# Kernel tuning notes

Hardware: AMD Instinct MI355X
Metric: run time of the kernel (lower is better)

## Reference

```python
import jax, jax.numpy as jnp
import numpy as np

DIM = 512
HEADS = 8
DIM_HEAD = 64
INNER = HEADS * DIM_HEAD


def setup_inputs() -> dict:
    key = jax.random.key(0)
    k1, k2, k3, k4 = jax.random.split(key, 4)
    x = jax.random.normal(k1, (4, 8192, DIM), dtype=jnp.float32)
    # nn.Linear(dim, inner*3, bias=False): weight applied as x @ W^T; store transposed form [dim, 3*inner]
    w_qkv = jax.random.normal(k2, (DIM, 3 * INNER), dtype=jnp.float32) / np.sqrt(DIM)
    w_out = jax.random.normal(k3, (INNER, DIM), dtype=jnp.float32) / np.sqrt(INNER)
    b_out = jax.random.normal(k4, (DIM,), dtype=jnp.float32) * 0.01
    return {"x": x, "w_qkv": w_qkv, "w_out": w_out, "b_out": b_out}


def reference(x, w_qkv, w_out, b_out):
    b, n, d = x.shape
    qkv = x @ w_qkv  # [b, n, 3*inner]
    q, k, v = jnp.split(qkv, 3, axis=-1)

    def to_heads(t):
        return t.reshape(b, n, HEADS, DIM_HEAD).transpose(0, 2, 1, 3)  # [b,h,n,dh]

    q, k, v = map(to_heads, (q, k, v))
    q = jax.nn.elu(q) + 1.0
    k = jax.nn.elu(k) + 1.0
    # kv summary: [b,h,dh,dh]
    kv = jnp.einsum('bhnd,bhnm->bhdm', k, v)
    # normalizer z: [b,h,n]  (note: original does NOT apply self.scale)
    z = 1.0 / (jnp.einsum('bhnd,bhd->bhn', q, k.sum(axis=2)) + 1e-6)
    out = jnp.einsum('bhnd,bhdm->bhnm', q, kv) * z[..., None]  # [b,h,n,dh]
    out = out.transpose(0, 2, 1, 3).reshape(b, n, INNER)
    return out @ w_out + b_out
```

## Files before the change

kernel.cpp:

```cpp
#include <hip/hip_runtime.h>
#include <hip/hip_bf16.h>

#define B_SZ 4
#define SEQ 8192
#define DIM 512
#define HEADS 8
#define DH 64
#define INNER 512
#define QKV_COLS 1536
#define M_TOT (B_SZ * SEQ)
#define BHN (B_SZ * HEADS)

typedef __bf16 bf16x8 __attribute__((ext_vector_type(8)));
typedef __bf16 bf16x4 __attribute__((ext_vector_type(4)));
typedef float f32x4 __attribute__((ext_vector_type(4)));

__device__ __forceinline__ float elu1(float x) {
    return x > 0.f ? x + 1.f : __expf(x);
}

__device__ __forceinline__ void gl_lds16(const void* g, void* l) {
    __builtin_amdgcn_global_load_lds(
        (const __attribute__((address_space(1))) unsigned int*)g,
        (__attribute__((address_space(3))) unsigned int*)l, 16, 0, 0);
}

__global__ void convert_all(const float* __restrict__ x,
                            const float* __restrict__ w_qkv,
                            const float* __restrict__ w_out,
                            __bf16* __restrict__ xb,
                            __bf16* __restrict__ wqkv_t,
                            __bf16* __restrict__ wout_t) {
    const int NX = M_TOT * DIM / 4;
    int id = blockIdx.x * 256 + threadIdx.x;
    if (id < NX) {
        float4 f = reinterpret_cast<const float4*>(x)[id];
        bf16x4 h = {(__bf16)f.x, (__bf16)f.y, (__bf16)f.z, (__bf16)f.w};
        reinterpret_cast<bf16x4*>(xb)[id] = h;
        return;
    }
    int id2 = id - NX;
    if (id2 < QKV_COLS * DIM) {
        int n = id2 / DIM, k = id2 % DIM;
        wqkv_t[id2] = (__bf16)w_qkv[k * QKV_COLS + n];
    } else {
        int id3 = id2 - QKV_COLS * DIM;
        if (id3 < INNER * DIM) {
            int n = id3 / DIM, k = id3 % DIM;
            wout_t[id3] = (__bf16)w_out[k * DIM + n];
        }
    }
}

#define TSTR 136
__launch_bounds__(256, 2)
__global__ void gemm_qkv(const __bf16* __restrict__ xb,
                         const __bf16* __restrict__ wqkv_t,
                         __bf16* __restrict__ q_ws,
                         __bf16* __restrict__ kT_ws,
                         __bf16* __restrict__ vT_ws) {
    __shared__ __attribute__((aligned(16))) char smem[128 * TSTR * 2];
    __bf16* As = (__bf16*)smem;
    __bf16* Bs = (__bf16*)(smem + 16384);
    __bf16* T  = (__bf16*)smem;

    const int tid = threadIdx.x;
    const int wid = tid >> 6;
    const int lane = tid & 63;
    const int wm = wid >> 1, wn = wid & 1;
    const int lq = lane >> 4, lr = lane & 15;
    const int m0 = blockIdx.x * 128;
    const int n0 = blockIdx.y * 128;
    const int lrow = lane >> 3;
    const int lsw  = ((lane & 7) ^ lrow) * 8;

    f32x4 acc[4][4] = {};

    for (int kb = 0; kb < DIM; kb += 64) {
#pragma unroll
        for (int t = 0; t < 4; ++t) {
            int qi = wid * 4 + t;
            int row = qi * 8 + lrow;
            gl_lds16(&xb[(size_t)(m0 + row) * DIM + kb + lsw], &As[qi * 512]);
            gl_lds16(&wqkv_t[(size_t)(n0 + row) * DIM + kb + lsw], &Bs[qi * 512]);
        }
        __syncthreads();
#pragma unroll
        for (int ks = 0; ks < 2; ++ks) {
            const int csw = ((ks * 4 + lq) ^ (lr & 7)) * 8;
            bf16x8 af[4], bfv[4];
#pragma unroll
            for (int i = 0; i < 4; ++i)
                af[i] = *reinterpret_cast<const bf16x8*>(
                    &As[(wm * 64 + i * 16 + lr) * 64 + csw]);
#pragma unroll
            for (int j = 0; j < 4; ++j)
                bfv[j] = *reinterpret_cast<const bf16x8*>(
                    &Bs[(wn * 64 + j * 16 + lr) * 64 + csw]);
#pragma unroll
            for (int i = 0; i < 4; ++i)
#pragma unroll
                for (int j = 0; j < 4; ++j)
                    acc[i][j] = __builtin_amdgcn_mfma_f32_16x16x32_bf16(
                        af[i], bfv[j], acc[i][j], 0, 0, 0);
        }
        __syncthreads();
    }

    const int which = n0 / INNER;
    const int n0w = n0 % INNER;
    const int b = m0 / SEQ;
    const int nbase = m0 % SEQ;

    if (which == 0) {
#pragma unroll
        for (int i = 0; i < 4; ++i)
#pragma unroll
            for (int j = 0; j < 4; ++j) {
                int col = wn * 64 + j * 16 + lr;
#pragma unroll
                for (int r = 0; r < 4; ++r)
                    T[(wm * 64 + i * 16 + lq * 4 + r) * TSTR + col] =
                        (__bf16)elu1(acc[i][j][r]);
            }
        __syncthreads();
#pragma unroll
        for (int it = 0; it < 8; ++it) {
            int c = tid + it * 256;
            int row = c >> 4, dc = (c & 15) * 8;
            bf16x8 v = *reinterpret_cast<const bf16x8*>(&T[row * TSTR + dc]);
            int col = n0w + dc;
            int h = col >> 6, d = col & 63;
            *reinterpret_cast<bf16x8*>(
                &q_ws[(((size_t)(b * HEADS + h)) * SEQ + nbase + row) * DH + d]) = v;
        }
    } else {
        __bf16* dst = (which == 1) ? kT_ws : vT_ws;
#pragma unroll
        for (int i = 0; i < 4; ++i)
#pragma unroll
            for (int j = 0; j < 4; ++j) {
                int col = wn * 64 + j * 16 + lr;
                int rowb = wm * 64 + i * 16 + lq * 4;
                bf16x4 h4;
#pragma unroll
                for (int r = 0; r < 4; ++r) {
                    float v = acc[i][j][r];
                    h4[r] = (__bf16)((which == 1) ? elu1(v) : v);
                }
                *reinterpret_cast<bf16x4*>(&T[col * TSTR + rowb]) = h4;
            }
        __syncthreads();
#pragma unroll
        for (int it = 0; it < 8; ++it) {
            int c = tid + it * 256;
            int colIdx = c >> 4, rc = (c & 15) * 8;
            bf16x8 v = *reinterpret_cast<const bf16x8*>(&T[colIdx * TSTR + rc]);
            int gcol = n0w + colIdx;
            int h = gcol >> 6, d = gcol & 63;
            *reinterpret_cast<bf16x8*>(
                &dst[(((size_t)(b * HEADS + h)) * DH + d) * SEQ + nbase + rc]) = v;
        }
    }
}

__launch_bounds__(256, 2)
__global__ void kv_reduce(const __bf16* __restrict__ kT,
                          const __bf16* __restrict__ vT,
                          float* __restrict__ kv_t,
                          float* __restrict__ ksum) {
    __shared__ __attribute__((aligned(16))) __bf16 Ks[64][136];
    __shared__ __attribute__((aligned(16))) __bf16 Vs[64][136];
    const int tid = threadIdx.x;
    const int wid = tid >> 6;
    const int lane = tid & 63;
    const int lq = lane >> 4, lr = lane & 15;
    const int bh = blockIdx.y;
    const int n0 = blockIdx.x * 512;
    const size_t base = (size_t)bh * DH * SEQ;
    f32x4 acc[4] = {};
    f32x4 acc1 = {};
    bf16x8 ones8;
#pragma unroll
    for (int e = 0; e < 8; ++e) ones8[e] = (__bf16)1.f;

    for (int ch = 0; ch < 4; ++ch) {
        int nc = n0 + ch * 128;
#pragma unroll
        for (int t = 0; t < 4; ++t) {
            int c = tid + t * 256;
            int row = c >> 4, kc = (c & 15) * 8;
            *reinterpret_cast<bf16x8*>(&Ks[row][kc]) =
                *reinterpret_cast<const bf16x8*>(&kT[base + (size_t)row * SEQ + nc + kc]);
            *reinterpret_cast<bf16x8*>(&Vs[row][kc]) =
                *reinterpret_cast<const bf16x8*>(&vT[base + (size_t)row * SEQ + nc + kc]);
        }
        __syncthreads();
#pragma unroll
        for (int ks = 0; ks < 4; ++ks) {
            bf16x8 a = *reinterpret_cast<const bf16x8*>(&Ks[wid * 16 + lr][ks * 32 + lq * 8]);
            acc1 = __builtin_amdgcn_mfma_f32_16x16x32_bf16(a, ones8, acc1, 0, 0, 0);
#pragma unroll
            for (int j = 0; j < 4; ++j) {
                bf16x8 b = *reinterpret_cast<const bf16x8*>(&Vs[j * 16 + lr][ks * 32 + lq * 8]);
                acc[j] = __builtin_amdgcn_mfma_f32_16x16x32_bf16(a, b, acc[j], 0, 0, 0);
            }
        }
        __syncthreads();
    }
    float* dst = kv_t + (size_t)bh * DH * DH;
#pragma unroll
    for (int j = 0; j < 4; ++j) {
        int m = j * 16 + lr;
#pragma unroll
        for (int r = 0; r < 4; ++r) {
            int d = wid * 16 + lq * 4 + r;
            atomicAdd(&dst[m * DH + d], acc[j][r]);
        }
    }
    if (lr == 0) {
#pragma unroll
        for (int r = 0; r < 4; ++r)
            atomicAdd(&ksum[bh * DH + wid * 16 + lq * 4 + r], acc1[r]);
    }
}

__launch_bounds__(256, 2)
__global__ void attn_kernel(const __bf16* __restrict__ q_ws,
                            const float* __restrict__ kv_t,
                            const float* __restrict__ ksum,
                            __bf16* __restrict__ attn) {
    __shared__ __attribute__((aligned(16))) __bf16 Qs[128][72];
    __shared__ __attribute__((aligned(16))) __bf16 KVs[64][72];
    __shared__ float zs[128];
    __shared__ float ks_s[64];
    const int tid = threadIdx.x;
    const int wid = tid >> 6, lane = tid & 63;
    const int lq = lane >> 4, lr = lane & 15;
    const int bh = blockIdx.y;
    const int b = bh >> 3, h = bh & 7;
    const int n0 = blockIdx.x * 128;
    const size_t qbase = ((size_t)bh * SEQ + n0) * DH;

#pragma unroll
    for (int t = 0; t < 4; ++t) {
        int c = tid + t * 256;
        int row = c >> 3, kc = (c & 7) * 8;
        *reinterpret_cast<bf16x8*>(&Qs[row][kc]) =
            *reinterpret_cast<const bf16x8*>(&q_ws[qbase + (size_t)row * DH + kc]);
    }
    const float* kvsrc = kv_t + (size_t)bh * DH * DH;
#pragma unroll
    for (int t = 0; t < 4; ++t) {
        int c = tid + t * 256;
        int m = c >> 4, dc = (c & 15) * 4;
        float4 f = *reinterpret_cast<const float4*>(&kvsrc[m * DH + dc]);
        bf16x4 h4 = {(__bf16)f.x, (__bf16)f.y, (__bf16)f.z, (__bf16)f.w};
        *reinterpret_cast<bf16x4*>(&KVs[m][dc]) = h4;
    }
    if (tid < 64) ks_s[tid] = ksum[bh * DH + tid];
    __syncthreads();
    {
        int row = tid >> 1, part = tid & 1;
        float s = 0.f;
#pragma unroll
        for (int j = 0; j < 32; ++j)
            s += (float)Qs[row][part * 32 + j] * ks_s[part * 32 + j];
        s += __shfl_xor(s, 1, 64);
        if (part == 0) zs[row] = 1.f / (s + 1e-6f);
    }
    __syncthreads();

    f32x4 acc[2][4] = {};
#pragma unroll
    for (int ks = 0; ks < 2; ++ks) {
        bf16x8 a0 = *reinterpret_cast<const bf16x8*>(&Qs[wid * 32 + lr][ks * 32 + lq * 8]);
        bf16x8 a1 = *reinterpret_cast<const bf16x8*>(&Qs[wid * 32 + 16 + lr][ks * 32 + lq * 8]);
#pragma unroll
        for (int j = 0; j < 4; ++j) {
            bf16x8 bfr = *reinterpret_cast<const bf16x8*>(&KVs[j * 16 + lr][ks * 32 + lq * 8]);
            acc[0][j] = __builtin_amdgcn_mfma_f32_16x16x32_bf16(a0, bfr, acc[0][j], 0, 0, 0);
            acc[1][j] = __builtin_amdgcn_mfma_f32_16x16x32_bf16(a1, bfr, acc[1][j], 0, 0, 0);
        }
    }
    __syncthreads();
#pragma unroll
    for (int mt = 0; mt < 2; ++mt)
#pragma unroll
        for (int j = 0; j < 4; ++j) {
            int m = j * 16 + lr;
#pragma unroll
            for (int r = 0; r < 4; ++r) {
                int row = wid * 32 + mt * 16 + lq * 4 + r;
                Qs[row][m] = (__bf16)(acc[mt][j][r] * zs[row]);
            }
        }
    __syncthreads();
#pragma unroll
    for (int it = 0; it < 4; ++it) {
        int c = tid + it * 256;
        int row = c >> 3, mc = (c & 7) * 8;
        bf16x8 v = *reinterpret_cast<const bf16x8*>(&Qs[row][mc]);
        *reinterpret_cast<bf16x8*>(
            &attn[((size_t)(b * SEQ + n0 + row)) * INNER + h * DH + mc]) = v;
    }
}

__launch_bounds__(256, 2)
__global__ void gemm_out(const __bf16* __restrict__ attn,
                         const __bf16* __restrict__ wout_t,
                         const float* __restrict__ b_out,
                         float* __restrict__ out) {
    __shared__ __attribute__((aligned(16))) char smem[32768];
    __bf16* As = (__bf16*)smem;
    __bf16* Bs = (__bf16*)(smem + 16384);

    const int tid = threadIdx.x;
    const int wid = tid >> 6;
    const int lane = tid & 63;
    const int wm = wid >> 1, wn = wid & 1;
    const int lq = lane >> 4, lr = lane & 15;
    const int m0 = blockIdx.x * 128;
    const int n0 = blockIdx.y * 128;
    const int lrow = lane >> 3;
    const int lsw  = ((lane & 7) ^ lrow) * 8;

    f32x4 acc[4][4] = {};

    for (int kb = 0; kb < INNER; kb += 64) {
#pragma unroll
        for (int t = 0; t < 4; ++t) {
            int qi = wid * 4 + t;
            int row = qi * 8 + lrow;
            gl_lds16(&attn[(size_t)(m0 + row) * INNER + kb + lsw], &As[qi * 512]);
            gl_lds16(&wout_t[(size_t)(n0 + row) * INNER + kb + lsw], &Bs[qi * 512]);
        }
        __syncthreads();
#pragma unroll
        for (int ks = 0; ks < 2; ++ks) {
            const int csw = ((ks * 4 + lq) ^ (lr & 7)) * 8;
            bf16x8 af[4], bfv[4];
#pragma unroll
            for (int i = 0; i < 4; ++i)
                af[i] = *reinterpret_cast<const bf16x8*>(
                    &As[(wm * 64 + i * 16 + lr) * 64 + csw]);
#pragma unroll
            for (int j = 0; j < 4; ++j)
                bfv[j] = *reinterpret_cast<const bf16x8*>(
                    &Bs[(wn * 64 + j * 16 + lr) * 64 + csw]);
#pragma unroll
            for (int i = 0; i < 4; ++i)
#pragma unroll
                for (int j = 0; j < 4; ++j)
                    acc[i][j] = __builtin_amdgcn_mfma_f32_16x16x32_bf16(
                        af[i], bfv[j], acc[i][j], 0, 0, 0);
        }
        __syncthreads();
    }

#pragma unroll
    for (int j = 0; j < 4; ++j) {
        int col = n0 + wn * 64 + j * 16 + lr;
        float bias = b_out[col];
#pragma unroll
        for (int i = 0; i < 4; ++i) {
            int row = m0 + wm * 64 + i * 16 + lq * 4;
#pragma unroll
            for (int r = 0; r < 4; ++r)
                out[(size_t)(row + r) * DIM + col] = acc[i][j][r] + bias;
        }
    }
}

extern "C" void kernel_launch(void* const* d_in, const int* in_sizes, int n_in,
                              void* d_out, int out_size, void* d_ws, size_t ws_size,
                              hipStream_t stream) {
    (void)in_sizes; (void)n_in; (void)out_size; (void)ws_size;
    const float* x     = (const float*)d_in[0];
    const float* w_qkv = (const float*)d_in[1];
    const float* w_out = (const float*)d_in[2];
    const float* b_out = (const float*)d_in[3];
    float* out = (float*)d_out;

    char* ws = (char*)d_ws;
    size_t off = 0;
    auto alloc = [&](size_t bytes) {
        char* p = ws + off;
        off += (bytes + 255) & ~(size_t)255;
        return p;
    };
    __bf16* xb     = (__bf16*)alloc((size_t)M_TOT * DIM * 2);
    __bf16* attn   = xb;
    __bf16* q_ws   = (__bf16*)alloc((size_t)BHN * SEQ * DH * 2);
    __bf16* kT_ws  = (__bf16*)alloc((size_t)BHN * SEQ * DH * 2);
    __bf16* vT_ws  = (__bf16*)alloc((size_t)BHN * SEQ * DH * 2);
    float*  kv_t   = (float*)alloc((size_t)BHN * DH * DH * 4 + (size_t)BHN * DH * 4);
    float*  ksum   = kv_t + (size_t)BHN * DH * DH;
    __bf16* wqkv_t = (__bf16*)alloc((size_t)QKV_COLS * DIM * 2);
    __bf16* wout_t = (__bf16*)alloc((size_t)INNER * DIM * 2);

    hipMemsetAsync(kv_t, 0, (size_t)BHN * DH * DH * 4 + (size_t)BHN * DH * 4, stream);
    convert_all<<<dim3(M_TOT * DIM / 4 / 256 + (QKV_COLS * DIM + INNER * DIM) / 256),
                  256, 0, stream>>>(x, w_qkv, w_out, xb, wqkv_t, wout_t);
    gemm_qkv<<<dim3(M_TOT / 128, QKV_COLS / 128), 256, 0, stream>>>(
        xb, wqkv_t, q_ws, kT_ws, vT_ws);
    kv_reduce<<<dim3(16, BHN), 256, 0, stream>>>(kT_ws, vT_ws, kv_t, ksum);
    attn_kernel<<<dim3(SEQ / 128, BHN), 256, 0, stream>>>(q_ws, kv_t, ksum, attn);
    gemm_out<<<dim3(M_TOT / 128, DIM / 128), 256, 0, stream>>>(attn, wout_t, b_out, out);
}
```

Before: 284.2 us.

## Rewrite QKV and output GEMMs as 256x256 double-buffered pipelined tiles

```diff
diff --git a/kernel.cpp b/kernel.cpp
--- a/kernel.cpp
+++ b/kernel.cpp
@@ -24,6 +24,9 @@
         (const __attribute__((address_space(1))) unsigned int*)g,
         (__attribute__((address_space(3))) unsigned int*)l, 16, 0, 0);
 }
+
+#define MFMA16(a, b, c) __builtin_amdgcn_mfma_f32_16x16x32_bf16(a, b, c, 0, 0, 0)
+#define BARRIER() asm volatile("s_barrier" ::: "memory")
 
 __global__ void convert_all(const float* __restrict__ x,
                             const float* __restrict__ w_qkv,
@@ -52,114 +55,229 @@
     }
 }
 
+__device__ __forceinline__ void gemm256_core(
+    const __bf16* __restrict__ Am, const __bf16* __restrict__ Bm,
+    int m0, int n0, char* smem, f32x4 acc[8][4])
+{
+    const int tid = threadIdx.x;
+    const int wid = tid >> 6;
+    const int lane = tid & 63;
+    const int wm = wid >> 2, wn = wid & 3;
+    const int lq = lane >> 4, lr = lane & 15;
+    const int lrow = lane >> 3;
+    const int lsw  = ((lane & 7) ^ lrow) * 8;
+
+    __bf16* const As0 = (__bf16*)smem;
+    __bf16* const Bs0 = (__bf16*)(smem + 32768);
+    __bf16* const As1 = (__bf16*)(smem + 65536);
+    __bf16* const Bs1 = (__bf16*)(smem + 98304);
+
+    const int csw0 = ((0 + lq) ^ (lr & 7)) * 8;
+    const int csw1 = ((4 + lq) ^ (lr & 7)) * 8;
+
+    auto stageB = [&](__bf16* Bs, int kt, int u) {
+        gl_lds16(&Bm[(size_t)(n0 + u * 64 + wid * 8 + lrow) * 512 + kt * 64 + lsw],
+                 Bs + (u * 64 + wid * 8) * 64);
+    };
+    auto stageA = [&](__bf16* As, int kt, int s2) {
+        int gr = (wid < 4) ? (s2 * 32 + wid * 8) : (128 + s2 * 32 + (wid - 4) * 8);
+        gl_lds16(&Am[(size_t)(m0 + gr + lrow) * 512 + kt * 64 + lsw],
+                 As + gr * 64);
+    };
+    auto ldA = [&](const __bf16* As, int m, int csw) -> bf16x8 {
+        return *reinterpret_cast<const bf16x8*>(As + (wm * 128 + m * 16 + lr) * 64 + csw);
+    };
+    auto ldB = [&](const __bf16* Bs, int n, int csw) -> bf16x8 {
+        return *reinterpret_cast<const bf16x8*>(Bs + (wn * 64 + n * 16 + lr) * 64 + csw);
+    };
+
+    stageB(Bs0, 0, 0); stageB(Bs0, 0, 1); stageB(Bs0, 0, 2); stageB(Bs0, 0, 3);
+    stageA(As0, 0, 0); stageA(As0, 0, 1); stageA(As0, 0, 2); stageA(As0, 0, 3);
+    asm volatile("s_waitcnt vmcnt(3)" ::: "memory");
+    BARRIER();
+
+#pragma unroll 2
+    for (int t = 0; t < 8; ++t) {
+        __bf16* const As  = (t & 1) ? As1 : As0;
+        __bf16* const Bs  = (t & 1) ? Bs1 : Bs0;
+        __bf16* const Asn = (t & 1) ? As0 : As1;
+        __bf16* const Bsn = (t & 1) ? Bs0 : Bs1;
+        const bool pf = (t < 7);
+        bf16x8 bfr[4][2];
+
+        {
+            bf16x8 a00 = ldA(As, 0, csw0), a01 = ldA(As, 0, csw1);
+            bf16x8 a10 = ldA(As, 1, csw0), a11 = ldA(As, 1, csw1);
+#pragma unroll
+            for (int n = 0; n < 4; ++n) { bfr[n][0] = ldB(Bs, n, csw0); bfr[n][1] = ldB(Bs, n, csw1); }
+            if (pf) { stageB(Bsn, t + 1, 0); stageB(Bsn, t + 1, 1); }
+            __builtin_amdgcn_s_setprio(1);
+#pragma unroll
+            for (int n = 0; n < 4; ++n) {
+                acc[0][n] = MFMA16(a00, bfr[n][0], acc[0][n]);
+                acc[0][n] = MFMA16(a01, bfr[n][1], acc[0][n]);
+                acc[1][n] = MFMA16(a10, bfr[n][0], acc[1][n]);
+                acc[1][n] = MFMA16(a11, bfr[n][1], acc[1][n]);
+            }
+            __builtin_amdgcn_s_setprio(0);
+            if (pf) asm volatile("s_waitcnt vmcnt(4)" ::: "memory");
+            else    asm volatile("s_waitcnt vmcnt(2)" ::: "memory");
+            BARRIER();
+        }
+        {
+            bf16x8 a00 = ldA(As, 2, csw0), a01 = ldA(As, 2, csw1);
+            bf16x8 a10 = ldA(As, 3, csw0), a11 = ldA(As, 3, csw1);
+            if (pf) { stageB(Bsn, t + 1, 2); stageB(Bsn, t + 1, 3); }
+            __builtin_amdgcn_s_setprio(1);
+#pragma unroll
+            for (int n = 0; n < 4; ++n) {
+                acc[2][n] = MFMA16(a00, bfr[n][0], acc[2][n]);
+                acc[2][n] = MFMA16(a01, bfr[n][1], acc[2][n]);
+                acc[3][n] = MFMA16(a10, bfr[n][0], acc[3][n]);
+                acc[3][n] = MFMA16(a11, bfr[n][1], acc[3][n]);
+            }
+            __builtin_amdgcn_s_setprio(0);
+            if (pf) asm volatile("s_waitcnt vmcnt(5)" ::: "memory");
+            else    asm volatile("s_waitcnt vmcnt(1)" ::: "memory");
+            BARRIER();
+        }
+        {
+            bf16x8 a00 = ldA(As, 4, csw0), a01 = ldA(As, 4, csw1);
+            bf16x8 a10 = ldA(As, 5, csw0), a11 = ldA(As, 5, csw1);
+            if (pf) { stageA(Asn, t + 1, 0); stageA(Asn, t + 1, 1); }
+            __builtin_amdgcn_s_setprio(1);
+#pragma unroll
+            for (int n = 0; n < 4; ++n) {
+                acc[4][n] = MFMA16(a00, bfr[n][0], acc[4][n]);
+                acc[4][n] = MFMA16(a01, bfr[n][1], acc[4][n]);
+                acc[5][n] = MFMA16(a10, bfr[n][0], acc[5][n]);
+                acc[5][n] = MFMA16(a11, bfr[n][1], acc[5][n]);
+            }
+            __builtin_amdgcn_s_setprio(0);
+            if (pf) asm volatile("s_waitcnt vmcnt(6)" ::: "memory");
+            else    asm volatile("s_waitcnt vmcnt(0)" ::: "memory");
+            BARRIER();
+        }
+        {
+            bf16x8 a00 = ldA(As, 6, csw0), a01 = ldA(As, 6, csw1);
+            bf16x8 a10 = ldA(As, 7, csw0), a11 = ldA(As, 7, csw1);
+            if (pf) { stageA(Asn, t + 1, 2); stageA(Asn, t + 1, 3); }
+            __builtin_amdgcn_s_setprio(1);
+#pragma unroll
+            for (int n = 0; n < 4; ++n) {
+                acc[6][n] = MFMA16(a00, bfr[n][0], acc[6][n]);
+                acc[6][n] = MFMA16(a01, bfr[n][1], acc[6][n]);
+                acc[7][n] = MFMA16(a10, bfr[n][0], acc[7][n]);
+                acc[7][n] = MFMA16(a11, bfr[n][1], acc[7][n]);
+            }
+            __builtin_amdgcn_s_setprio(0);
+            if (pf) asm volatile("s_waitcnt vmcnt(3)" ::: "memory");
+            BARRIER();
+        }
+    }
+}
+
 #define TSTR 136
-__launch_bounds__(256, 2)
+__launch_bounds__(512, 2)
 __global__ void gemm_qkv(const __bf16* __restrict__ xb,
                          const __bf16* __restrict__ wqkv_t,
                          __bf16* __restrict__ q_ws,
                          __bf16* __restrict__ kT_ws,
                          __bf16* __restrict__ vT_ws) {
-    __shared__ __attribute__((aligned(16))) char smem[128 * TSTR * 2];
-    __bf16* As = (__bf16*)smem;
-    __bf16* Bs = (__bf16*)(smem + 16384);
-    __bf16* T  = (__bf16*)smem;
+    __shared__ __attribute__((aligned(16))) char smem[131072];
+    const int f  = blockIdx.y * gridDim.x + blockIdx.x;
+    const int xc = f & 7, sl = f >> 3;
+    const int m0 = (xc * 16 + sl / 6) * 256;
+    const int n0 = (sl % 6) * 256;
+
+    f32x4 acc[8][4] = {};
+    gemm256_core(xb, wqkv_t, m0, n0, smem, acc);
 
     const int tid = threadIdx.x;
     const int wid = tid >> 6;
     const int lane = tid & 63;
-    const int wm = wid >> 1, wn = wid & 1;
+    const int wm = wid >> 2, wn = wid & 3;
     const int lq = lane >> 4, lr = lane & 15;
-    const int m0 = blockIdx.x * 128;
-    const int n0 = blockIdx.y * 128;
-    const int lrow = lane >> 3;
-    const int lsw  = ((lane & 7) ^ lrow) * 8;
-
-    f32x4 acc[4][4] = {};
-
-    for (int kb = 0; kb < DIM; kb += 64) {
-#pragma unroll
-        for (int t = 0; t < 4; ++t) {
-            int qi = wid * 4 + t;
-            int row = qi * 8 + lrow;
-            gl_lds16(&xb[(size_t)(m0 + row) * DIM + kb + lsw], &As[qi * 512]);
-            gl_lds16(&wqkv_t[(size_t)(n0 + row) * DIM + kb + lsw], &Bs[qi * 512]);
-        }
-        __syncthreads();
-#pragma unroll
-        for (int ks = 0; ks < 2; ++ks) {
-            const int csw = ((ks * 4 + lq) ^ (lr & 7)) * 8;
-            bf16x8 af[4], bfv[4];
-#pragma unroll
-            for (int i = 0; i < 4; ++i)
-                af[i] = *reinterpret_cast<const bf16x8*>(
-                    &As[(wm * 64 + i * 16 + lr) * 64 + csw]);
-#pragma unroll
-            for (int j = 0; j < 4; ++j)
-                bfv[j] = *reinterpret_cast<const bf16x8*>(
-                    &Bs[(wn * 64 + j * 16 + lr) * 64 + csw]);
-#pragma unroll
-            for (int i = 0; i < 4; ++i)
-#pragma unroll
-                for (int j = 0; j < 4; ++j)
-                    acc[i][j] = __builtin_amdgcn_mfma_f32_16x16x32_bf16(
-                        af[i], bfv[j], acc[i][j], 0, 0, 0);
-        }
-        __syncthreads();
-    }
 
     const int which = n0 / INNER;
     const int n0w = n0 % INNER;
     const int b = m0 / SEQ;
     const int nbase = m0 % SEQ;
 
+    __bf16* const T0 = (__bf16*)smem;
+    __bf16* const T1 = (__bf16*)(smem + 34816);
+
     if (which == 0) {
 #pragma unroll
-        for (int i = 0; i < 4; ++i)
-#pragma unroll
-            for (int j = 0; j < 4; ++j) {
-                int col = wn * 64 + j * 16 + lr;
-#pragma unroll
-                for (int r = 0; r < 4; ++r)
-                    T[(wm * 64 + i * 16 + lq * 4 + r) * TSTR + col] =
-                        (__bf16)elu1(acc[i][j][r]);
-            }
-        __syncthreads();
-#pragma unroll
-        for (int it = 0; it < 8; ++it) {
-            int c = tid + it * 256;
-            int row = c >> 4, dc = (c & 15) * 8;
-            bf16x8 v = *reinterpret_cast<const bf16x8*>(&T[row * TSTR + dc]);
-            int col = n0w + dc;
-            int h = col >> 6, d = col & 63;
-            *reinterpret_cast<bf16x8*>(
-                &q_ws[(((size_t)(b * HEADS + h)) * SEQ + nbase + row) * DH + d]) = v;
+        for (int rh = 0; rh < 2; ++rh) {
+            if (wm == rh) {
+#pragma unroll
+                for (int m = 0; m < 8; ++m)
+#pragma unroll
+                    for (int n = 0; n < 4; ++n) {
+                        int col = wn * 64 + n * 16 + lr;
+                        __bf16* Tb = (wn * 64 + n * 16 < 128) ? T0 : T1;
+                        int cl = col & 127;
+#pragma unroll
+                        for (int r = 0; r < 4; ++r)
+                            Tb[(m * 16 + lq * 4 + r) * TSTR + cl] =
+                                (__bf16)elu1(acc[m][n][r]);
+                    }
+            }
+            __syncthreads();
+#pragma unroll
+            for (int it = 0; it < 8; ++it) {
+                int cch = tid + it * 512;
+                int row = cch >> 5;
+                int cc = (cch & 31) * 8;
+                const __bf16* Tb = (cc < 128) ? T0 : T1;
+                int dc = cc & 127;
+                bf16x8 v = *reinterpret_cast<const bf16x8*>(&Tb[row * TSTR + dc]);
+                int colg = n0w + cc;
+                int h = colg >> 6, d = colg & 63;
+                *reinterpret_cast<bf16x8*>(
+                    &q_ws[(((size_t)(b * HEADS + h)) * SEQ + nbase + rh * 128 + row) * DH + d]) = v;
+            }
+            __syncthreads();
         }
     } else {
         __bf16* dst = (which == 1) ? kT_ws : vT_ws;
 #pragma unroll
-        for (int i = 0; i < 4; ++i)
-#pragma unroll
-            for (int j = 0; j < 4; ++j) {
-                int col = wn * 64 + j * 16 + lr;
-                int rowb = wm * 64 + i * 16 + lq * 4;
-                bf16x4 h4;
-#pragma unroll
-                for (int r = 0; r < 4; ++r) {
-                    float v = acc[i][j][r];
-                    h4[r] = (__bf16)((which == 1) ? elu1(v) : v);
+        for (int rh = 0; rh < 2; ++rh) {
+            if (wm == rh) {
+#pragma unroll
+                for (int m = 0; m < 8; ++m) {
+                    int rowb = m * 16 + lq * 4;
+#pragma unroll
+                    for (int n = 0; n < 4; ++n) {
+                        int col = wn * 64 + n * 16 + lr;
+                        __bf16* Tb = (wn * 64 + n * 16 < 128) ? T0 : T1;
+                        int cl = col & 127;
+                        bf16x4 h4;
+#pragma unroll
+                        for (int r = 0; r < 4; ++r) {
+                            float v = acc[m][n][r];
+                            h4[r] = (__bf16)((which == 1) ? elu1(v) : v);
+                        }
+                        *reinterpret_cast<bf16x4*>(&Tb[cl * TSTR + rowb]) = h4;
+                    }
                 }
-                *reinterpret_cast<bf16x4*>(&T[col * TSTR + rowb]) = h4;
-            }
-        __syncthreads();
-#pragma unroll
-        for (int it = 0; it < 8; ++it) {
-            int c = tid + it * 256;
-            int colIdx = c >> 4, rc = (c & 15) * 8;
-            bf16x8 v = *reinterpret_cast<const bf16x8*>(&T[colIdx * TSTR + rc]);
-            int gcol = n0w + colIdx;
-            int h = gcol >> 6, d = gcol & 63;
-            *reinterpret_cast<bf16x8*>(
-                &dst[(((size_t)(b * HEADS + h)) * DH + d) * SEQ + nbase + rc]) = v;
+            }
+            __syncthreads();
+#pragma unroll
+            for (int it = 0; it < 8; ++it) {
+                int cch = tid + it * 512;
+                int colIdx = cch >> 4;
+                int rc = (cch & 15) * 8;
+                const __bf16* Tb = (colIdx < 128) ? T0 : T1;
+                int cl = colIdx & 127;
+                bf16x8 v = *reinterpret_cast<const bf16x8*>(&Tb[cl * TSTR + rc]);
+                int g = n0w + colIdx;
+                int h = g >> 6, d = g & 63;
+                *reinterpret_cast<bf16x8*>(
+                    &dst[(((size_t)(b * HEADS + h)) * DH + d) * SEQ + nbase + rh * 128 + rc]) = v;
+            }
+            __syncthreads();
         }
     }
 }
@@ -199,11 +317,11 @@
 #pragma unroll
         for (int ks = 0; ks < 4; ++ks) {
             bf16x8 a = *reinterpret_cast<const bf16x8*>(&Ks[wid * 16 + lr][ks * 32 + lq * 8]);
-            acc1 = __builtin_amdgcn_mfma_f32_16x16x32_bf16(a, ones8, acc1, 0, 0, 0);
+            acc1 = MFMA16(a, ones8, acc1);
 #pragma unroll
             for (int j = 0; j < 4; ++j) {
                 bf16x8 b = *reinterpret_cast<const bf16x8*>(&Vs[j * 16 + lr][ks * 32 + lq * 8]);
-                acc[j] = __builtin_amdgcn_mfma_f32_16x16x32_bf16(a, b, acc[j], 0, 0, 0);
+                acc[j] = MFMA16(a, b, acc[j]);
             }
         }
         __syncthreads();
@@ -279,8 +397,8 @@
 #pragma unroll
         for (int j = 0; j < 4; ++j) {
             bf16x8 bfr = *reinterpret_cast<const bf16x8*>(&KVs[j * 16 + lr][ks * 32 + lq * 8]);
-            acc[0][j] = __builtin_amdgcn_mfma_f32_16x16x32_bf16(a0, bfr, acc[0][j], 0, 0, 0);
-            acc[1][j] = __builtin_amdgcn_mfma_f32_16x16x32_bf16(a1, bfr, acc[1][j], 0, 0, 0);
+            acc[0][j] = MFMA16(a0, bfr, acc[0][j]);
+            acc[1][j] = MFMA16(a1, bfr, acc[1][j]);
         }
     }
     __syncthreads();
@@ -306,68 +424,36 @@
     }
 }
 
-__launch_bounds__(256, 2)
+__launch_bounds__(512, 2)
 __global__ void gemm_out(const __bf16* __restrict__ attn,
                          const __bf16* __restrict__ wout_t,
                          const float* __restrict__ b_out,
                          float* __restrict__ out) {
-    __shared__ __attribute__((aligned(16))) char smem[32768];
-    __bf16* As = (__bf16*)smem;
-    __bf16* Bs = (__bf16*)(smem + 16384);
+    __shared__ __attribute__((aligned(16))) char smem[131072];
+    const int f  = blockIdx.y * gridDim.x + blockIdx.x;
+    const int xc = f & 7, sl = f >> 3;
+    const int m0 = (xc * 16 + (sl >> 1)) * 256;
+    const int n0 = (sl & 1) * 256;
+
+    f32x4 acc[8][4] = {};
+    gemm256_core(attn, wout_t, m0, n0, smem, acc);
 
     const int tid = threadIdx.x;
     const int wid = tid >> 6;
     const int lane = tid & 63;
-    const int wm = wid >> 1, wn = wid & 1;
+    const int wm = wid >> 2, wn = wid & 3;
     const int lq = lane >> 4, lr = lane & 15;
-    const int m0 = blockIdx.x * 128;
-    const int n0 = blockIdx.y * 128;
-    const int lrow = lane >> 3;
-    const int lsw  = ((lane & 7) ^ lrow) * 8;
-
-    f32x4 acc[4][4] = {};
-
-    for (int kb = 0; kb < INNER; kb += 64) {
-#pragma unroll
-        for (int t = 0; t < 4; ++t) {
-            int qi = wid * 4 + t;
-            int row = qi * 8 + lrow;
-            gl_lds16(&attn[(size_t)(m0 + row) * INNER + kb + lsw], &As[qi * 512]);
-            gl_lds16(&wout_t[(size_t)(n0 + row) * INNER + kb + lsw], &Bs[qi * 512]);
-        }
-        __syncthreads();
-#pragma unroll
-        for (int ks = 0; ks < 2; ++ks) {
-            const int csw = ((ks * 4 + lq) ^ (lr & 7)) * 8;
-            bf16x8 af[4], bfv[4];
-#pragma unroll
-            for (int i = 0; i < 4; ++i)
-                af[i] = *reinterpret_cast<const bf16x8*>(
-                    &As[(wm * 64 + i * 16 + lr) * 64 + csw]);
-#pragma unroll
-            for (int j = 0; j < 4; ++j)
-                bfv[j] = *reinterpret_cast<const bf16x8*>(
-                    &Bs[(wn * 64 + j * 16 + lr) * 64 + csw]);
-#pragma unroll
-            for (int i = 0; i < 4; ++i)
-#pragma unroll
-                for (int j = 0; j < 4; ++j)
-                    acc[i][j] = __builtin_amdgcn_mfma_f32_16x16x32_bf16(
-                        af[i], bfv[j], acc[i][j], 0, 0, 0);
-        }
-        __syncthreads();
-    }
-
-#pragma unroll
-    for (int j = 0; j < 4; ++j) {
-        int col = n0 + wn * 64 + j * 16 + lr;
+
+#pragma unroll
+    for (int n = 0; n < 4; ++n) {
+        int col = n0 + wn * 64 + n * 16 + lr;
         float bias = b_out[col];
 #pragma unroll
-        for (int i = 0; i < 4; ++i) {
-            int row = m0 + wm * 64 + i * 16 + lq * 4;
+        for (int m = 0; m < 8; ++m) {
+            int row = m0 + wm * 128 + m * 16 + lq * 4;
 #pragma unroll
             for (int r = 0; r < 4; ++r)
-                out[(size_t)(row + r) * DIM + col] = acc[i][j][r] + bias;
+                out[(size_t)(row + r) * DIM + col] = acc[m][n][r] + bias;
         }
     }
 }
@@ -402,9 +488,9 @@
     hipMemsetAsync(kv_t, 0, (size_t)BHN * DH * DH * 4 + (size_t)BHN * DH * 4, stream);
     convert_all<<<dim3(M_TOT * DIM / 4 / 256 + (QKV_COLS * DIM + INNER * DIM) / 256),
                   256, 0, stream>>>(x, w_qkv, w_out, xb, wqkv_t, wout_t);
-    gemm_qkv<<<dim3(M_TOT / 128, QKV_COLS / 128), 256, 0, stream>>>(
+    gemm_qkv<<<dim3(M_TOT / 256, QKV_COLS / 256), 512, 0, stream>>>(
         xb, wqkv_t, q_ws, kT_ws, vT_ws);
     kv_reduce<<<dim3(16, BHN), 256, 0, stream>>>(kT_ws, vT_ws, kv_t, ksum);
     attn_kernel<<<dim3(SEQ / 128, BHN), 256, 0, stream>>>(q_ws, kv_t, ksum, attn);
-    gemm_out<<<dim3(M_TOT / 128, DIM / 128), 256, 0, stream>>>(attn, wout_t, b_out, out);
-}
+    gemm_out<<<dim3(M_TOT / 256, DIM / 256), 512, 0, stream>>>(attn, wout_t, b_out, out);
+}
```

After: 269.5 us. 1.05x faster.

## Fuse attention apply with output projection in one per-row-tile kernel

Applied to the files above, without the earlier changes.

```diff
diff --git a/kernel.cpp b/kernel.cpp
--- a/kernel.cpp
+++ b/kernel.cpp
@@ -24,6 +24,8 @@
         (const __attribute__((address_space(1))) unsigned int*)g,
         (__attribute__((address_space(3))) unsigned int*)l, 16, 0, 0);
 }
+
+#define MFMA16(a, b, c) __builtin_amdgcn_mfma_f32_16x16x32_bf16(a, b, c, 0, 0, 0)
 
 __global__ void convert_all(const float* __restrict__ x,
                             const float* __restrict__ w_qkv,
@@ -101,8 +103,7 @@
             for (int i = 0; i < 4; ++i)
 #pragma unroll
                 for (int j = 0; j < 4; ++j)
-                    acc[i][j] = __builtin_amdgcn_mfma_f32_16x16x32_bf16(
-                        af[i], bfv[j], acc[i][j], 0, 0, 0);
+                    acc[i][j] = MFMA16(af[i], bfv[j], acc[i][j]);
         }
         __syncthreads();
     }
@@ -199,11 +200,11 @@
 #pragma unroll
         for (int ks = 0; ks < 4; ++ks) {
             bf16x8 a = *reinterpret_cast<const bf16x8*>(&Ks[wid * 16 + lr][ks * 32 + lq * 8]);
-            acc1 = __builtin_amdgcn_mfma_f32_16x16x32_bf16(a, ones8, acc1, 0, 0, 0);
+            acc1 = MFMA16(a, ones8, acc1);
 #pragma unroll
             for (int j = 0; j < 4; ++j) {
                 bf16x8 b = *reinterpret_cast<const bf16x8*>(&Vs[j * 16 + lr][ks * 32 + lq * 8]);
-                acc[j] = __builtin_amdgcn_mfma_f32_16x16x32_bf16(a, b, acc[j], 0, 0, 0);
+                acc[j] = MFMA16(a, b, acc[j]);
             }
         }
         __syncthreads();
@@ -225,149 +226,132 @@
     }
 }
 
-__launch_bounds__(256, 2)
-__global__ void attn_kernel(const __bf16* __restrict__ q_ws,
-                            const float* __restrict__ kv_t,
-                            const float* __restrict__ ksum,
-                            __bf16* __restrict__ attn) {
-    __shared__ __attribute__((aligned(16))) __bf16 Qs[128][72];
-    __shared__ __attribute__((aligned(16))) __bf16 KVs[64][72];
+__launch_bounds__(512, 2)
+__global__ void attn_out(const __bf16* __restrict__ q_ws,
+                         const float* __restrict__ kv_t,
+                         const float* __restrict__ ksum,
+                         const __bf16* __restrict__ wout_t,
+                         const float* __restrict__ b_out,
+                         float* __restrict__ out) {
+    __shared__ __attribute__((aligned(16))) __bf16 kvs[2][64 * 64];
+    __shared__ __attribute__((aligned(16))) __bf16 attn_lds[128 * 64];
     __shared__ float zs[128];
-    __shared__ float ks_s[64];
+
     const int tid = threadIdx.x;
     const int wid = tid >> 6, lane = tid & 63;
     const int lq = lane >> 4, lr = lane & 15;
-    const int bh = blockIdx.y;
-    const int b = bh >> 3, h = bh & 7;
-    const int n0 = blockIdx.x * 128;
-    const size_t qbase = ((size_t)bh * SEQ + n0) * DH;
-
-#pragma unroll
-    for (int t = 0; t < 4; ++t) {
-        int c = tid + t * 256;
-        int row = c >> 3, kc = (c & 7) * 8;
-        *reinterpret_cast<bf16x8*>(&Qs[row][kc]) =
-            *reinterpret_cast<const bf16x8*>(&q_ws[qbase + (size_t)row * DH + kc]);
-    }
-    const float* kvsrc = kv_t + (size_t)bh * DH * DH;
-#pragma unroll
-    for (int t = 0; t < 4; ++t) {
-        int c = tid + t * 256;
-        int m = c >> 4, dc = (c & 15) * 4;
-        float4 f = *reinterpret_cast<const float4*>(&kvsrc[m * DH + dc]);
-        bf16x4 h4 = {(__bf16)f.x, (__bf16)f.y, (__bf16)f.z, (__bf16)f.w};
-        *reinterpret_cast<bf16x4*>(&KVs[m][dc]) = h4;
-    }
-    if (tid < 64) ks_s[tid] = ksum[bh * DH + tid];
+    const int wm = wid >> 2, wn = wid & 3;
+    const int m0 = blockIdx.x * 128;
+    const int b = m0 / SEQ;
+    const int nseq = m0 % SEQ;
+
+    f32x4 acc[4][8] = {};
+
+    auto stage_kv = [&](int buf, int h) {
+        int m = tid >> 3, c0 = tid & 7;
+        const float* src = &kv_t[(((size_t)(b * 8 + h)) * 64 + m) * 64 + c0 * 8];
+        float4 f0 = *reinterpret_cast<const float4*>(src);
+        float4 f1 = *reinterpret_cast<const float4*>(src + 4);
+        bf16x8 v = {(__bf16)f0.x, (__bf16)f0.y, (__bf16)f0.z, (__bf16)f0.w,
+                    (__bf16)f1.x, (__bf16)f1.y, (__bf16)f1.z, (__bf16)f1.w};
+        *reinterpret_cast<bf16x8*>(&kvs[buf][m * 64 + ((c0 ^ (m & 7)) * 8)]) = v;
+    };
+
+    stage_kv(0, 0);
     __syncthreads();
-    {
-        int row = tid >> 1, part = tid & 1;
-        float s = 0.f;
-#pragma unroll
-        for (int j = 0; j < 32; ++j)
-            s += (float)Qs[row][part * 32 + j] * ks_s[part * 32 + j];
-        s += __shfl_xor(s, 1, 64);
-        if (part == 0) zs[row] = 1.f / (s + 1e-6f);
-    }
-    __syncthreads();
-
-    f32x4 acc[2][4] = {};
-#pragma unroll
-    for (int ks = 0; ks < 2; ++ks) {
-        bf16x8 a0 = *reinterpret_cast<const bf16x8*>(&Qs[wid * 32 + lr][ks * 32 + lq * 8]);
-        bf16x8 a1 = *reinterpret_cast<const bf16x8*>(&Qs[wid * 32 + 16 + lr][ks * 32 + lq * 8]);
-#pragma unroll
-        for (int j = 0; j < 4; ++j) {
-            bf16x8 bfr = *reinterpret_cast<const bf16x8*>(&KVs[j * 16 + lr][ks * 32 + lq * 8]);
-            acc[0][j] = __builtin_amdgcn_mfma_f32_16x16x32_bf16(a0, bfr, acc[0][j], 0, 0, 0);
-            acc[1][j] = __builtin_amdgcn_mfma_f32_16x16x32_bf16(a1, bfr, acc[1][j], 0, 0, 0);
-        }
-    }
-    __syncthreads();
-#pragma unroll
-    for (int mt = 0; mt < 2; ++mt)
-#pragma unroll
-        for (int j = 0; j < 4; ++j) {
-            int m = j * 16 + lr;
-#pragma unroll
-            for (int r = 0; r < 4; ++r) {
-                int row = wid * 32 + mt * 16 + lq * 4 + r;
-                Qs[row][m] = (__bf16)(acc[mt][j][r] * zs[row]);
+
+    for (int h = 0; h < 8; ++h) {
+        const int buf = h & 1;
+        const size_t qb = (((size_t)(b * 8 + h)) * SEQ + nseq) * DH;
+
+        {
+            int row = tid >> 2, part = tid & 3;
+            const __bf16* qp = &q_ws[qb + (size_t)row * DH + part * 16];
+            bf16x8 v0 = *reinterpret_cast<const bf16x8*>(qp);
+            bf16x8 v1 = *reinterpret_cast<const bf16x8*>(qp + 8);
+            const float* kp = &ksum[(b * 8 + h) * 64 + part * 16];
+            float s = 0.f;
+#pragma unroll
+            for (int j = 0; j < 8; ++j) s += (float)v0[j] * kp[j];
+#pragma unroll
+            for (int j = 0; j < 8; ++j) s += (float)v1[j] * kp[8 + j];
+            s += __shfl_xor(s, 1, 64);
+            s += __shfl_xor(s, 2, 64);
+            if (part == 0) zs[row] = 1.f / (s + 1e-6f);
+        }
+
+        {
+            const int r0 = wid * 16;
+            bf16x8 qa[2];
+#pragma unroll
+            for (int ks = 0; ks < 2; ++ks)
+                qa[ks] = *reinterpret_cast<const bf16x8*>(
+                    &q_ws[qb + (size_t)(r0 + lr) * DH + ks * 32 + lq * 8]);
+            f32x4 acc1[4] = {};
+#pragma unroll
+            for (int ks = 0; ks < 2; ++ks)
+#pragma unroll
+                for (int j = 0; j < 4; ++j) {
+                    int mr = j * 16 + lr;
+                    bf16x8 bk = *reinterpret_cast<const bf16x8*>(
+                        &kvs[buf][mr * 64 + (((ks * 4 + lq) ^ (mr & 7)) * 8)]);
+                    acc1[j] = MFMA16(qa[ks], bk, acc1[j]);
+                }
+            asm volatile("s_waitcnt lgkmcnt(0)" ::: "memory");
+            float zr[4];
+#pragma unroll
+            for (int r = 0; r < 4; ++r) zr[r] = zs[r0 + lq * 4 + r];
+#pragma unroll
+            for (int j = 0; j < 4; ++j)
+#pragma unroll
+                for (int r = 0; r < 4; ++r) {
+                    int row = r0 + lq * 4 + r;
+                    int chk = j * 2 + (lr >> 3);
+                    attn_lds[row * 64 + ((chk ^ (row & 7)) * 8) + (lr & 7)] =
+                        (__bf16)(acc1[j][r] * zr[r]);
+                }
+        }
+        if (h < 7) stage_kv(buf ^ 1, h + 1);
+        __syncthreads();
+
+        {
+            bf16x8 af[4][2];
+#pragma unroll
+            for (int i = 0; i < 4; ++i)
+#pragma unroll
+                for (int ks = 0; ks < 2; ++ks) {
+                    int arow = wm * 64 + i * 16 + lr;
+                    af[i][ks] = *reinterpret_cast<const bf16x8*>(
+                        &attn_lds[arow * 64 + (((ks * 4 + lq) ^ (arow & 7)) * 8)]);
+                }
+#pragma unroll
+            for (int n = 0; n < 8; ++n) {
+                int c = wn * 128 + n * 16 + lr;
+                const __bf16* wp = &wout_t[(size_t)c * 512 + h * 64 + lq * 8];
+                bf16x8 bw0 = *reinterpret_cast<const bf16x8*>(wp);
+                bf16x8 bw1 = *reinterpret_cast<const bf16x8*>(wp + 32);
+                __builtin_amdgcn_s_setprio(1);
+#pragma unroll
+                for (int i = 0; i < 4; ++i) {
+                    acc[i][n] = MFMA16(af[i][0], bw0, acc[i][n]);
+                    acc[i][n] = MFMA16(af[i][1], bw1, acc[i][n]);
+                }
+                __builtin_amdgcn_s_setprio(0);
             }
         }
-    __syncthreads();
-#pragma unroll
-    for (int it = 0; it < 4; ++it) {
-        int c = tid + it * 256;
-        int row = c >> 3, mc = (c & 7) * 8;
-        bf16x8 v = *reinterpret_cast<const bf16x8*>(&Qs[row][mc]);
-        *reinterpret_cast<bf16x8*>(
-            &attn[((size_t)(b * SEQ + n0 + row)) * INNER + h * DH + mc]) = v;
-    }
-}
-
-__launch_bounds__(256, 2)
-__global__ void gemm_out(const __bf16* __restrict__ attn,
-                         const __bf16* __restrict__ wout_t,
-                         const float* __restrict__ b_out,
-                         float* __restrict__ out) {
-    __shared__ __attribute__((aligned(16))) char smem[32768];
-    __bf16* As = (__bf16*)smem;
-    __bf16* Bs = (__bf16*)(smem + 16384);
-
-    const int tid = threadIdx.x;
-    const int wid = tid >> 6;
-    const int lane = tid & 63;
-    const int wm = wid >> 1, wn = wid & 1;
-    const int lq = lane >> 4, lr = lane & 15;
-    const int m0 = blockIdx.x * 128;
-    const int n0 = blockIdx.y * 128;
-    const int lrow = lane >> 3;
-    const int lsw  = ((lane & 7) ^ lrow) * 8;
-
-    f32x4 acc[4][4] = {};
-
-    for (int kb = 0; kb < INNER; kb += 64) {
-#pragma unroll
-        for (int t = 0; t < 4; ++t) {
-            int qi = wid * 4 + t;
-            int row = qi * 8 + lrow;
-            gl_lds16(&attn[(size_t)(m0 + row) * INNER + kb + lsw], &As[qi * 512]);
-            gl_lds16(&wout_t[(size_t)(n0 + row) * INNER + kb + lsw], &Bs[qi * 512]);
-        }
-        __syncthreads();
-#pragma unroll
-        for (int ks = 0; ks < 2; ++ks) {
-            const int csw = ((ks * 4 + lq) ^ (lr & 7)) * 8;
-            bf16x8 af[4], bfv[4];
-#pragma unroll
-            for (int i = 0; i < 4; ++i)
-                af[i] = *reinterpret_cast<const bf16x8*>(
-                    &As[(wm * 64 + i * 16 + lr) * 64 + csw]);
-#pragma unroll
-            for (int j = 0; j < 4; ++j)
-                bfv[j] = *reinterpret_cast<const bf16x8*>(
-                    &Bs[(wn * 64 + j * 16 + lr) * 64 + csw]);
-#pragma unroll
-            for (int i = 0; i < 4; ++i)
-#pragma unroll
-                for (int j = 0; j < 4; ++j)
-                    acc[i][j] = __builtin_amdgcn_mfma_f32_16x16x32_bf16(
-                        af[i], bfv[j], acc[i][j], 0, 0, 0);
-        }
-        __syncthreads();
-    }
-
-#pragma unroll
-    for (int j = 0; j < 4; ++j) {
-        int col = n0 + wn * 64 + j * 16 + lr;
+        __syncthreads();
+    }
+
+#pragma unroll
+    for (int n = 0; n < 8; ++n) {
+        int col = wn * 128 + n * 16 + lr;
         float bias = b_out[col];
 #pragma unroll
         for (int i = 0; i < 4; ++i) {
             int row = m0 + wm * 64 + i * 16 + lq * 4;
 #pragma unroll
             for (int r = 0; r < 4; ++r)
-                out[(size_t)(row + r) * DIM + col] = acc[i][j][r] + bias;
+                out[(size_t)(row + r) * DIM + col] = acc[i][n][r] + bias;
         }
     }
 }
@@ -390,7 +374,6 @@
         return p;
     };
     __bf16* xb     = (__bf16*)alloc((size_t)M_TOT * DIM * 2);
-    __bf16* attn   = xb;
     __bf16* q_ws   = (__bf16*)alloc((size_t)BHN * SEQ * DH * 2);
     __bf16* kT_ws  = (__bf16*)alloc((size_t)BHN * SEQ * DH * 2);
     __bf16* vT_ws  = (__bf16*)alloc((size_t)BHN * SEQ * DH * 2);
@@ -405,6 +388,6 @@
     gemm_qkv<<<dim3(M_TOT / 128, QKV_COLS / 128), 256, 0, stream>>>(
         xb, wqkv_t, q_ws, kT_ws, vT_ws);
     kv_reduce<<<dim3(16, BHN), 256, 0, stream>>>(kT_ws, vT_ws, kv_t, ksum);
-    attn_kernel<<<dim3(SEQ / 128, BHN), 256, 0, stream>>>(q_ws, kv_t, ksum, attn);
-    gemm_out<<<dim3(M_TOT / 128, DIM / 128), 256, 0, stream>>>(attn, wout_t, b_out, out);
-}
+    attn_out<<<dim3(M_TOT / 128), 512, 0, stream>>>(
+        q_ws, kv_t, ksum, wout_t, b_out, out);
+}
```

Result: slower. 293.7 us (+3.3%).
